# Kernel tuning notes

Hardware: AMD Instinct MI355X
Metric: run time of the kernel (lower is better)

## Reference

```python
import jax, jax.numpy as jnp
import numpy as np

B = 2048          # batch
D = 256           # agent input dim
S = 32            # num_splines
CANVAS = 128      # canvas_size
NUM_T = 50        # samples along each Bezier curve (hard-coded in module)
BRUSH = 1         # brush_size (hard-coded)
SCALE = 1e-4      # Normal scale hard-coded in forward (log_std is unused)
W_STAMP = -0.07   # per-stamp weight (hard-coded)
BG = 0.3          # background_shade


def setup_inputs() -> dict:
    key = jax.random.key(0)
    k1, k2 = jax.random.split(key, 2)
    x = jax.random.normal(k1, (B, D), dtype=jnp.float32)
    W_agent = jax.random.normal(k2, (D, S * 6), dtype=jnp.float32) * 0.05
    b_agent = jnp.zeros((S * 6,), dtype=jnp.float32)
    return {"x": x, "W_agent": W_agent, "b_agent": b_agent}


def _paint_multiple_splines(sample):
    # sample: [B, S*6] in (0,1)
    bsz = sample.shape[0]
    params = sample.reshape(bsz, -1, 6) * CANVAS          # [B, S, 6]
    P0 = params[..., 0:2][:, :, None, :]                   # [B, S, 1, 2]
    P1 = params[..., 2:4][:, :, None, :]
    P2 = params[..., 4:6][:, :, None, :]
    t = jnp.linspace(0.0, 1.0, NUM_T, dtype=params.dtype).reshape(1, 1, NUM_T, 1)
    # quadratic Bezier: [B, S, T, 2]
    spline_points = (1 - t) ** 2 * P0 + 2 * (1 - t) * t * P1 + t ** 2 * P2
    coords = jnp.round(spline_points).astype(jnp.int32)
    r = jnp.arange(-BRUSH, BRUSH + 1)
    dx, dy = jnp.meshgrid(r, r, indexing="ij")
    dx, dy = dx.ravel(), dy.ravel()                        # [9]
    x_idx = jnp.clip(coords[..., 0][..., None] + dx, 0, CANVAS - 1)  # [B,S,T,9]
    y_idx = jnp.clip(coords[..., 1][..., None] + dy, 0, CANVAS - 1)
    flat_idx = (x_idx * CANVAS + y_idx).reshape(bsz, -1)   # [B, S*T*9]
    weights = jnp.full(flat_idx.shape, W_STAMP, dtype=jnp.float32)
    canvas_flat = jnp.zeros((bsz, CANVAS * CANVAS), dtype=jnp.float32)
    canvas_flat = canvas_flat.at[jnp.arange(bsz)[:, None], flat_idx].add(weights)
    canvas = canvas_flat.reshape(bsz, CANVAS, CANVAS)
    return jnp.clip(canvas + BG, 0.0, 1.0)


def reference(x, W_agent, b_agent):
    mu = x @ W_agent + b_agent                             # [B, S*6]
    scale = jnp.float32(SCALE)
    log2pi = jnp.log(jnp.float32(2.0) * jnp.pi)
    dim = mu.shape[-1]
    # eval-time path: raw_sample = mu
    raw = mu
    log_prob = jnp.sum(
        -0.5 * ((raw - mu) / scale) ** 2 - jnp.log(scale) - 0.5 * log2pi,
        axis=-1,
    )                                                      # [B]
    entropy = jnp.full(
        (mu.shape[0],), dim * (0.5 + 0.5 * log2pi + jnp.log(scale)),
        dtype=jnp.float32,
    )                                                      # [B]
    sample = jax.nn.sigmoid(raw)                           # [B, S*6]
    sketch = _paint_multiple_splines(sample)               # [B, CANVAS, CANVAS]
    return sketch, log_prob, entropy, sample
```

## Files before the change

kernel.cpp:

```cpp
#include <hip/hip_runtime.h>
#include <math.h>

#define NB      2048
#define DIM     256
#define SC6     192
#define CV      128
#define NT      50
#define NBPB    4
#define CWORDS  (CV * CV / 4)

#define LPV  (1591.9491530441301f)
#define ENV  (-1495.9491530441301f)

#define SKETCH_N   ((size_t)NB * CV * CV)
#define LP_OFF     (SKETCH_N)
#define ENT_OFF    (LP_OFF + NB)
#define SAMPLE_OFF (ENT_OFF + NB)

typedef float vfloat4 __attribute__((ext_vector_type(4)));

__device__ __forceinline__ void barrier_lds_only() {
    asm volatile("s_waitcnt lgkmcnt(0)\n\ts_barrier" ::: "memory");
}

__device__ __forceinline__ void do_paint(
    unsigned int* __restrict__ cnv,
    const double (* __restrict__ spb)[32],
    const double* __restrict__ cfa, const double* __restrict__ cfb,
    const double* __restrict__ cfc, int tid)
{
    const int s = tid & 31;
    const double P0x = spb[0][s], P0y = spb[1][s];
    const double P1x = spb[2][s], P1y = spb[3][s];
    const double P2x = spb[4][s], P2y = spb[5][s];

    for (int i = tid; i < 32 * NT; i += 512) {
        int kraw = i >> 5;
        int k    = (kraw * 9) % 50;
        double a  = cfa[k];
        double bq = cfb[k];
        double c  = cfc[k];
        double px = a * P0x + bq * P1x + c * P2x;
        double py = a * P0y + bq * P1y + c * P2y;
        int cx = (int)rint(px);
        int cy = (int)rint(py);

        int y0 = min(max(cy - 1, 0), CV - 1);
        int y1 = min(max(cy,     0), CV - 1);
        int y2 = min(max(cy + 1, 0), CV - 1);
        int cb = y0 >> 2;
        unsigned incA = 1u << ((y0 & 3) << 3);
        unsigned incB = 0u;
        unsigned i1 = 1u << ((y1 & 3) << 3);
        unsigned i2 = 1u << ((y2 & 3) << 3);
        if ((y1 >> 2) == cb) incA += i1; else incB += i1;
        if ((y2 >> 2) == cb) incA += i2; else incB += i2;

        int x0 = min(max(cx - 1, 0), CV - 1);
        int x1 = min(max(cx,     0), CV - 1);
        int x2 = min(max(cx + 1, 0), CV - 1);
        int rows[3] = {x0, x1, x2};
        #pragma unroll
        for (int r = 0; r < 3; ++r) {
            int xi = rows[r];
            int base = xi << 5;
            atomicAdd(&cnv[base + ((cb + xi) & 31)], incA);
            if (incB) atomicAdd(&cnv[base + ((cb + 1 + xi) & 31)], incB);
        }
    }
}

__device__ __forceinline__ void do_epilogue(
    unsigned int* __restrict__ cnv, float* __restrict__ outb, int tid)
{
    vfloat4* ob = (vfloat4*)outb;
    for (int w = tid; w < CWORDS; w += 512) {
        int xi  = w >> 5;
        int idx = (xi << 5) + (((w & 31) + xi) & 31);
        unsigned v = cnv[idx];
        cnv[idx] = 0u;
        vfloat4 r;
        r.x = fminf(fmaxf(0.3f - 0.07f * (float)( v        & 255u), 0.0f), 1.0f);
        r.y = fminf(fmaxf(0.3f - 0.07f * (float)((v >>  8) & 255u), 0.0f), 1.0f);
        r.z = fminf(fmaxf(0.3f - 0.07f * (float)((v >> 16) & 255u), 0.0f), 1.0f);
        r.w = fminf(fmaxf(0.3f - 0.07f * (float)( v >> 24        ), 0.0f), 1.0f);
        ob[w] = r;
    }
}

__global__ __launch_bounds__(512) void fused_kernel(
    const float* __restrict__ x, const float* __restrict__ W,
    const float* __restrict__ bias, float* __restrict__ out)
{
    __shared__ unsigned int cnt[2][CWORDS];
    __shared__ double sp[NBPB][6][32];
    __shared__ double cfa[NT], cfb[NT], cfc[NT];

    const int b0  = blockIdx.x * NBPB;
    const int tid = threadIdx.x;

    if (tid < SC6) {
        const int j = tid;
        const float* xb = x + (size_t)b0 * DIM;
        double a0 = 0.0, a1 = 0.0, a2 = 0.0, a3 = 0.0;
        #pragma unroll 8
        for (int d = 0; d < DIM; ++d) {
            double wd = (double)W[d * SC6 + j];
            a0 = fma((double)xb[d],           wd, a0);
            a1 = fma((double)xb[DIM + d],     wd, a1);
            a2 = fma((double)xb[2 * DIM + d], wd, a2);
            a3 = fma((double)xb[3 * DIM + d], wd, a3);
        }
        double bj = (double)bias[j];
        double s0 = 1.0 / (1.0 + exp(-(a0 + bj)));
        double s1 = 1.0 / (1.0 + exp(-(a1 + bj)));
        double s2 = 1.0 / (1.0 + exp(-(a2 + bj)));
        double s3 = 1.0 / (1.0 + exp(-(a3 + bj)));
        out[SAMPLE_OFF + (size_t)b0 * SC6 + j]       = (float)s0;
        out[SAMPLE_OFF + (size_t)(b0 + 1) * SC6 + j] = (float)s1;
        out[SAMPLE_OFF + (size_t)(b0 + 2) * SC6 + j] = (float)s2;
        out[SAMPLE_OFF + (size_t)(b0 + 3) * SC6 + j] = (float)s3;
        sp[0][j % 6][j / 6] = s0 * 128.0;
        sp[1][j % 6][j / 6] = s1 * 128.0;
        sp[2][j % 6][j / 6] = s2 * 128.0;
        sp[3][j % 6][j / 6] = s3 * 128.0;
    } else {
        const int t2 = tid - SC6;
        uint4* c4 = (uint4*)&cnt[0][0];
        uint4 z = make_uint4(0u, 0u, 0u, 0u);
        for (int w = t2; w < 2048; w += 320) c4[w] = z;
        if (t2 < NT) {
            double t = (t2 == NT - 1) ? 1.0 : (double)t2 * (1.0 / 49.0);
            double u = 1.0 - t;
            cfa[t2] = u * u;
            cfb[t2] = (2.0 * u) * t;
            cfc[t2] = t * t;
        }
        if (t2 >= 56 && t2 < 60) out[LP_OFF  + b0 + (t2 - 56)] = LPV;
        if (t2 >= 60 && t2 < 64) out[ENT_OFF + b0 + (t2 - 60)] = ENV;
    }
    barrier_lds_only();

    #pragma unroll
    for (int bb = 0; bb < NBPB; ++bb) {
        if (bb > 0) {
            do_epilogue(cnt[(bb - 1) & 1],
                        out + (size_t)(b0 + bb - 1) * CV * CV, tid);
        }
        do_paint(cnt[bb & 1], sp[bb], cfa, cfb, cfc, tid);
        barrier_lds_only();
    }
    do_epilogue(cnt[(NBPB - 1) & 1],
                out + (size_t)(b0 + NBPB - 1) * CV * CV, tid);
}

extern "C" void kernel_launch(void* const* d_in, const int* in_sizes, int n_in,
                              void* d_out, int out_size, void* d_ws, size_t ws_size,
                              hipStream_t stream) {
    const float* x    = (const float*)d_in[0];
    const float* W    = (const float*)d_in[1];
    const float* bias = (const float*)d_in[2];
    float* out = (float*)d_out;

    fused_kernel<<<NB / NBPB, 512, 0, stream>>>(x, W, bias, out);
}
```

Before: 157.7 us.

## Switch to one batch row per 256-thread block, dropping double-buffered canvas pipeline

Each block now handles a single batch element with 256 threads and a single LDS canvas, rather than four elements per 512-thread block with a double-buffered canvas that overlapped painting with writeback. Shared memory per block shrinks, so more blocks can be resident per CU (launch bounds hint 6), and the grid grows to 2048 blocks. In exchange, W is reloaded per row instead of being reused across four rows in the GEMV, and the paint/epilogue overlap within a block is lost.

```diff
diff --git a/kernel.cpp b/kernel.cpp
--- a/kernel.cpp
+++ b/kernel.cpp
@@ -6,7 +6,6 @@
 #define SC6     192
 #define CV      128
 #define NT      50
-#define NBPB    4
 #define CWORDS  (CV * CV / 4)
 
 #define LPV  (1591.9491530441301f)
@@ -23,112 +22,35 @@
     asm volatile("s_waitcnt lgkmcnt(0)\n\ts_barrier" ::: "memory");
 }
 
-__device__ __forceinline__ void do_paint(
-    unsigned int* __restrict__ cnv,
-    const double (* __restrict__ spb)[32],
-    const double* __restrict__ cfa, const double* __restrict__ cfb,
-    const double* __restrict__ cfc, int tid)
-{
-    const int s = tid & 31;
-    const double P0x = spb[0][s], P0y = spb[1][s];
-    const double P1x = spb[2][s], P1y = spb[3][s];
-    const double P2x = spb[4][s], P2y = spb[5][s];
-
-    for (int i = tid; i < 32 * NT; i += 512) {
-        int kraw = i >> 5;
-        int k    = (kraw * 9) % 50;
-        double a  = cfa[k];
-        double bq = cfb[k];
-        double c  = cfc[k];
-        double px = a * P0x + bq * P1x + c * P2x;
-        double py = a * P0y + bq * P1y + c * P2y;
-        int cx = (int)rint(px);
-        int cy = (int)rint(py);
-
-        int y0 = min(max(cy - 1, 0), CV - 1);
-        int y1 = min(max(cy,     0), CV - 1);
-        int y2 = min(max(cy + 1, 0), CV - 1);
-        int cb = y0 >> 2;
-        unsigned incA = 1u << ((y0 & 3) << 3);
-        unsigned incB = 0u;
-        unsigned i1 = 1u << ((y1 & 3) << 3);
-        unsigned i2 = 1u << ((y2 & 3) << 3);
-        if ((y1 >> 2) == cb) incA += i1; else incB += i1;
-        if ((y2 >> 2) == cb) incA += i2; else incB += i2;
-
-        int x0 = min(max(cx - 1, 0), CV - 1);
-        int x1 = min(max(cx,     0), CV - 1);
-        int x2 = min(max(cx + 1, 0), CV - 1);
-        int rows[3] = {x0, x1, x2};
-        #pragma unroll
-        for (int r = 0; r < 3; ++r) {
-            int xi = rows[r];
-            int base = xi << 5;
-            atomicAdd(&cnv[base + ((cb + xi) & 31)], incA);
-            if (incB) atomicAdd(&cnv[base + ((cb + 1 + xi) & 31)], incB);
-        }
-    }
-}
-
-__device__ __forceinline__ void do_epilogue(
-    unsigned int* __restrict__ cnv, float* __restrict__ outb, int tid)
-{
-    vfloat4* ob = (vfloat4*)outb;
-    for (int w = tid; w < CWORDS; w += 512) {
-        int xi  = w >> 5;
-        int idx = (xi << 5) + (((w & 31) + xi) & 31);
-        unsigned v = cnv[idx];
-        cnv[idx] = 0u;
-        vfloat4 r;
-        r.x = fminf(fmaxf(0.3f - 0.07f * (float)( v        & 255u), 0.0f), 1.0f);
-        r.y = fminf(fmaxf(0.3f - 0.07f * (float)((v >>  8) & 255u), 0.0f), 1.0f);
-        r.z = fminf(fmaxf(0.3f - 0.07f * (float)((v >> 16) & 255u), 0.0f), 1.0f);
-        r.w = fminf(fmaxf(0.3f - 0.07f * (float)( v >> 24        ), 0.0f), 1.0f);
-        ob[w] = r;
-    }
-}
-
-__global__ __launch_bounds__(512) void fused_kernel(
+__global__ __launch_bounds__(256, 6) void fused_kernel(
     const float* __restrict__ x, const float* __restrict__ W,
     const float* __restrict__ bias, float* __restrict__ out)
 {
-    __shared__ unsigned int cnt[2][CWORDS];
-    __shared__ double sp[NBPB][6][32];
+    __shared__ unsigned int cnt[CWORDS];
+    __shared__ double sp[6][32];
     __shared__ double cfa[NT], cfb[NT], cfc[NT];
 
-    const int b0  = blockIdx.x * NBPB;
+    const int b   = blockIdx.x;
     const int tid = threadIdx.x;
 
     if (tid < SC6) {
         const int j = tid;
-        const float* xb = x + (size_t)b0 * DIM;
-        double a0 = 0.0, a1 = 0.0, a2 = 0.0, a3 = 0.0;
-        #pragma unroll 8
-        for (int d = 0; d < DIM; ++d) {
-            double wd = (double)W[d * SC6 + j];
-            a0 = fma((double)xb[d],           wd, a0);
-            a1 = fma((double)xb[DIM + d],     wd, a1);
-            a2 = fma((double)xb[2 * DIM + d], wd, a2);
-            a3 = fma((double)xb[3 * DIM + d], wd, a3);
+        const float* xb = x + (size_t)b * DIM;
+        double a0 = 0.0, a1 = 0.0;
+        #pragma unroll 4
+        for (int d = 0; d < DIM; d += 2) {
+            a0 = fma((double)xb[d],     (double)W[d * SC6 + j],       a0);
+            a1 = fma((double)xb[d + 1], (double)W[(d + 1) * SC6 + j], a1);
         }
-        double bj = (double)bias[j];
-        double s0 = 1.0 / (1.0 + exp(-(a0 + bj)));
-        double s1 = 1.0 / (1.0 + exp(-(a1 + bj)));
-        double s2 = 1.0 / (1.0 + exp(-(a2 + bj)));
-        double s3 = 1.0 / (1.0 + exp(-(a3 + bj)));
-        out[SAMPLE_OFF + (size_t)b0 * SC6 + j]       = (float)s0;
-        out[SAMPLE_OFF + (size_t)(b0 + 1) * SC6 + j] = (float)s1;
-        out[SAMPLE_OFF + (size_t)(b0 + 2) * SC6 + j] = (float)s2;
-        out[SAMPLE_OFF + (size_t)(b0 + 3) * SC6 + j] = (float)s3;
-        sp[0][j % 6][j / 6] = s0 * 128.0;
-        sp[1][j % 6][j / 6] = s1 * 128.0;
-        sp[2][j % 6][j / 6] = s2 * 128.0;
-        sp[3][j % 6][j / 6] = s3 * 128.0;
+        double s0 = 1.0 / (1.0 + exp(-((a0 + a1) + (double)bias[j])));
+        out[SAMPLE_OFF + (size_t)b * SC6 + j] = (float)s0;
+        sp[j % 6][j / 6] = s0 * 128.0;
     } else {
         const int t2 = tid - SC6;
-        uint4* c4 = (uint4*)&cnt[0][0];
+        uint4* c4 = (uint4*)cnt;
         uint4 z = make_uint4(0u, 0u, 0u, 0u);
-        for (int w = t2; w < 2048; w += 320) c4[w] = z;
+        #pragma unroll
+        for (int w = t2; w < CWORDS / 4; w += 64) c4[w] = z;
         if (t2 < NT) {
             double t = (t2 == NT - 1) ? 1.0 : (double)t2 * (1.0 / 49.0);
             double u = 1.0 - t;
@@ -136,22 +58,66 @@
             cfb[t2] = (2.0 * u) * t;
             cfc[t2] = t * t;
         }
-        if (t2 >= 56 && t2 < 60) out[LP_OFF  + b0 + (t2 - 56)] = LPV;
-        if (t2 >= 60 && t2 < 64) out[ENT_OFF + b0 + (t2 - 60)] = ENV;
+        if (t2 == 50) out[LP_OFF  + b] = LPV;
+        if (t2 == 51) out[ENT_OFF + b] = ENV;
     }
     barrier_lds_only();
 
-    #pragma unroll
-    for (int bb = 0; bb < NBPB; ++bb) {
-        if (bb > 0) {
-            do_epilogue(cnt[(bb - 1) & 1],
-                        out + (size_t)(b0 + bb - 1) * CV * CV, tid);
+    {
+        const int s = tid & 31;
+        const double P0x = sp[0][s], P0y = sp[1][s];
+        const double P1x = sp[2][s], P1y = sp[3][s];
+        const double P2x = sp[4][s], P2y = sp[5][s];
+
+        for (int i = tid; i < 32 * NT; i += 256) {
+            int kraw = i >> 5;
+            int k    = (kraw * 9) % 50;
+            double a  = cfa[k];
+            double bq = cfb[k];
+            double c  = cfc[k];
+            double px = a * P0x + bq * P1x + c * P2x;
+            double py = a * P0y + bq * P1y + c * P2y;
+            int cx = (int)rint(px);
+            int cy = (int)rint(py);
+
+            int y0 = min(max(cy - 1, 0), CV - 1);
+            int y1 = min(max(cy,     0), CV - 1);
+            int y2 = min(max(cy + 1, 0), CV - 1);
+            int cb = y0 >> 2;
+            unsigned incA = 1u << ((y0 & 3) << 3);
+            unsigned incB = 0u;
+            unsigned i1 = 1u << ((y1 & 3) << 3);
+            unsigned i2 = 1u << ((y2 & 3) << 3);
+            if ((y1 >> 2) == cb) incA += i1; else incB += i1;
+            if ((y2 >> 2) == cb) incA += i2; else incB += i2;
+
+            int x0 = min(max(cx - 1, 0), CV - 1);
+            int x1 = min(max(cx,     0), CV - 1);
+            int x2 = min(max(cx + 1, 0), CV - 1);
+            int rows[3] = {x0, x1, x2};
+            #pragma unroll
+            for (int r = 0; r < 3; ++r) {
+                int xi = rows[r];
+                int base = xi << 5;
+                atomicAdd(&cnt[base + ((cb + xi) & 31)], incA);
+                if (incB) atomicAdd(&cnt[base + ((cb + 1 + xi) & 31)], incB);
+            }
         }
-        do_paint(cnt[bb & 1], sp[bb], cfa, cfb, cfc, tid);
-        barrier_lds_only();
     }
-    do_epilogue(cnt[(NBPB - 1) & 1],
-                out + (size_t)(b0 + NBPB - 1) * CV * CV, tid);
+    barrier_lds_only();
+
+    vfloat4* ob = (vfloat4*)(out + (size_t)b * CV * CV);
+    for (int w = tid; w < CWORDS; w += 256) {
+        int xi  = w >> 5;
+        int idx = (xi << 5) + (((w & 31) + xi) & 31);
+        unsigned v = cnt[idx];
+        vfloat4 r;
+        r.x = fminf(fmaxf(0.3f - 0.07f * (float)( v         & 255u), 0.0f), 1.0f);
+        r.y = fminf(fmaxf(0.3f - 0.07f * (float)((v >>  8) & 255u), 0.0f), 1.0f);
+        r.z = fminf(fmaxf(0.3f - 0.07f * (float)((v >> 16) & 255u), 0.0f), 1.0f);
+        r.w = fminf(fmaxf(0.3f - 0.07f * (float)( v >> 24        ), 0.0f), 1.0f);
+        ob[w] = r;
+    }
 }
 
 extern "C" void kernel_launch(void* const* d_in, const int* in_sizes, int n_in,
@@ -162,5 +128,5 @@
     const float* bias = (const float*)d_in[2];
     float* out = (float*)d_out;
 
-    fused_kernel<<<NB / NBPB, 512, 0, stream>>>(x, W, bias, out);
+    fused_kernel<<<NB, 256, 0, stream>>>(x, W, bias, out);
 }
```

New measurement: 158.6 us. Within noise of the previous version (+0.6%).
